# Optimization experiments

Hardware: AMD Instinct MI355X
Metric: run time of the kernel (lower is better)

The kernel has to match this reference:

```python
import jax, jax.numpy as jnp
import numpy as np

N_NODES = 100000
N_EDGES = 1000000
IN_DIM = 64
OUT_DIM = 64
EDGE_DIM = 16
LN_EPS = 1e-5
GINE_EPS = 0.0  # PyG GINEConv default eps


def setup_inputs() -> dict:
    key = jax.random.key(0)
    ks = jax.random.split(key, 10)
    s = lambda d: 1.0 / np.sqrt(d)
    x = jax.random.normal(ks[0], (N_NODES, IN_DIM), dtype=jnp.float32)
    edge_index = jax.random.randint(ks[1], (2, N_EDGES), 0, N_NODES, dtype=jnp.int64)
    edge_attr = jax.random.normal(ks[2], (N_EDGES, EDGE_DIM), dtype=jnp.float32)
    # GINEConv internal edge projection Linear(edge_dim, in_dim)
    We = jax.random.uniform(ks[3], (EDGE_DIM, IN_DIM), jnp.float32, -s(EDGE_DIM), s(EDGE_DIM))
    be = jax.random.uniform(ks[4], (IN_DIM,), jnp.float32, -s(EDGE_DIM), s(EDGE_DIM))
    # MLP: Linear(in_dim, out_dim) -> ReLU -> Linear(out_dim, out_dim)
    W1 = jax.random.uniform(ks[5], (IN_DIM, OUT_DIM), jnp.float32, -s(IN_DIM), s(IN_DIM))
    b1 = jax.random.uniform(ks[6], (OUT_DIM,), jnp.float32, -s(IN_DIM), s(IN_DIM))
    W2 = jax.random.uniform(ks[7], (OUT_DIM, OUT_DIM), jnp.float32, -s(OUT_DIM), s(OUT_DIM))
    b2 = jax.random.uniform(ks[8], (OUT_DIM,), jnp.float32, -s(OUT_DIM), s(OUT_DIM))
    ln_gamma = jnp.ones((OUT_DIM,), jnp.float32)
    ln_beta = jnp.zeros((OUT_DIM,), jnp.float32)
    return {"x": x, "edge_index": edge_index, "edge_attr": edge_attr,
            "We": We, "be": be, "W1": W1, "b1": b1, "W2": W2, "b2": b2,
            "ln_gamma": ln_gamma, "ln_beta": ln_beta}


def reference(x, edge_index, edge_attr, We, be, W1, b1, W2, b2, ln_gamma, ln_beta):
    src, dst = edge_index[0], edge_index[1]
    # message: ReLU(x_j + lin(edge_attr))  [E, IN_DIM]
    msg = jax.nn.relu(x[src] + edge_attr @ We + be)
    # scatter-sum into target nodes  [N, IN_DIM]
    aggr = jax.ops.segment_sum(msg, dst, num_segments=x.shape[0])
    h = (1.0 + GINE_EPS) * x + aggr
    # MLP
    h = jax.nn.relu(h @ W1 + b1) @ W2 + b2
    # LayerNorm over last dim
    mu = jnp.mean(h, axis=-1, keepdims=True)
    var = jnp.var(h, axis=-1, keepdims=True)
    h = (h - mu) * jax.lax.rsqrt(var + LN_EPS) * ln_gamma + ln_beta
    return jax.nn.relu(h)
```

## Files before the change

kernel.cpp:

```cpp
#include <hip/hip_runtime.h>

typedef short short8 __attribute__((ext_vector_type(8)));
typedef float f32x4 __attribute__((ext_vector_type(4)));

__device__ __forceinline__ float bf2f(unsigned short b) {
    union { unsigned u; float f; } c;
    c.u = ((unsigned)b) << 16;
    return c.f;
}

__device__ __forceinline__ unsigned short f2bf(float x) {
    union { float f; unsigned u; } c;
    c.f = x;
    unsigned u = c.u;
    u += 0x7fffu + ((u >> 16) & 1u);
    return (unsigned short)(u >> 16);
}

__device__ __forceinline__ float loadf(const void* p, long long i, unsigned isbf) {
    if (isbf) return bf2f(((const unsigned short*)p)[i]);
    return ((const float*)p)[i];
}

__device__ __forceinline__ f32x4 mfma16(short8 a, short8 b, f32x4 c) {
    return __builtin_amdgcn_mfma_f32_16x16x32_bf16(a, b, c, 0, 0, 0);
}

__global__ void gine_flag_kernel(const unsigned* gm_bits, const unsigned* ei_bits,
                                 unsigned* flags) {
    if (blockIdx.x == 0 && threadIdx.x == 0) {
        flags[0] = (gm_bits[0] == 0x3F803F80u) ? 1u : 0u;
        unsigned o = 0;
        for (int k = 0; k < 8; ++k) o |= ei_bits[2 * k + 1];
        flags[1] = (o == 0u) ? 1u : 0u;
    }
}

__global__ void gine_zero_kernel(float* p, int n) {
    int t = blockIdx.x * blockDim.x + threadIdx.x;
    if (t < n) p[t] = 0.0f;
}

__global__ void gine_prep_kernel(const void* W1, const void* b1,
                                 const void* W2, const void* b2,
                                 const void* gm, const void* bt,
                                 const void* We, const void* be,
                                 const unsigned* flags,
                                 unsigned short* W1B, unsigned short* W2B,
                                 float* vecs) {
    int t = blockIdx.x * blockDim.x + threadIdx.x;
    unsigned isbf = flags[0];
    if (t < 8192) {
        int which = t >> 12;
        int u = t & 4095;
        int j = u & 7, L = (u >> 3) & 63, ktnt = u >> 9;
        int kt = ktnt >> 2, nt = ktnt & 3;
        int k = kt * 32 + (L >> 4) * 8 + j;
        int c = nt * 16 + (L & 15);
        const void* W = which ? W2 : W1;
        unsigned short v = f2bf(loadf(W, k * 64 + c, isbf));
        if (which) W2B[u] = v; else W1B[u] = v;
    } else if (t < 8448) {
        int u = t - 8192;
        const void* s = (u < 64) ? b1 : (u < 128) ? b2 : (u < 192) ? gm : bt;
        vecs[u] = loadf(s, u & 63, isbf);
    } else if (t < 8512) {
        vecs[256 + (t - 8448)] = loadf(be, t - 8448, isbf);
    } else if (t < 9536) {
        int u = t - 8512;
        vecs[320 + u] = loadf(We, u, isbf);
    }
}

__global__ void gine_hist_kernel(const void* edge_index, const unsigned* flags,
                                 int* count, int E, int N) {
    int t = blockIdx.x * blockDim.x + threadIdx.x;
    int stride = gridDim.x * blockDim.x;
    unsigned is64 = flags[1];
    for (int e = t; e < E; e += stride) {
        long long dst = is64 ? ((const long long*)edge_index)[E + e]
                             : (long long)((const int*)edge_index)[E + e];
        if (dst >= 0 && dst < N) atomicAdd(&count[(int)dst], 1);
    }
}

__global__ void gine_scan1_kernel(const int* count, int* row_start, int* bsum,
                                  int N) {
    __shared__ int s[256];
    int t = threadIdx.x;
    int i = blockIdx.x * 256 + t;
    int v = (i < N) ? count[i] : 0;
    s[t] = v;
    __syncthreads();
    for (int off = 1; off < 256; off <<= 1) {
        int u = (t >= off) ? s[t - off] : 0;
        __syncthreads();
        s[t] += u;
        __syncthreads();
    }
    if (i < N) row_start[i] = s[t] - v;
    if (t == 255) bsum[blockIdx.x] = s[255];
}

__global__ void gine_scan2_kernel(int* bsum, int* bscan, int* row_start,
                                  int nb, int N) {
    __shared__ int s[512];
    int t = threadIdx.x;
    int v = (t < nb) ? bsum[t] : 0;
    s[t] = v;
    __syncthreads();
    for (int off = 1; off < 512; off <<= 1) {
        int u = (t >= off) ? s[t - off] : 0;
        __syncthreads();
        s[t] += u;
        __syncthreads();
    }
    if (t < nb) bscan[t] = s[t] - v;
    if (t == nb - 1) row_start[N] = s[t];
}

__global__ void gine_scan3_kernel(int* row_start, int* cursor,
                                  const int* bscan, int N) {
    int i = blockIdx.x * 256 + threadIdx.x;
    if (i < N) {
        int r = row_start[i] + bscan[blockIdx.x];
        row_start[i] = r;
        cursor[i] = r;
    }
}

__global__ void gine_scatter_kernel(const void* edge_index, const unsigned* flags,
                                    int* cursor, unsigned long long* sorted,
                                    int E, int N) {
    int t = blockIdx.x * blockDim.x + threadIdx.x;
    int stride = gridDim.x * blockDim.x;
    unsigned is64 = flags[1];
    for (int e = t; e < E; e += stride) {
        long long src, dst;
        if (is64) {
            src = ((const long long*)edge_index)[e];
            dst = ((const long long*)edge_index)[E + e];
        } else {
            src = ((const int*)edge_index)[e];
            dst = ((const int*)edge_index)[E + e];
        }
        if (dst < 0 || dst >= N) continue;
        if (src < 0) src = 0;
        if (src >= N) src = N - 1;
        int pos = atomicAdd(&cursor[(int)dst], 1);
        sorted[pos] = ((unsigned long long)(unsigned)e << 32) | (unsigned long long)(unsigned)src;
    }
}

__global__ void gine_gather_kernel(const void* x, const void* edge_attr,
                                   const unsigned long long* sorted,
                                   const int* row_start, const float* vecs,
                                   const unsigned* flags, float* h, int N) {
    int w = threadIdx.x >> 6;
    int lane = threadIdx.x & 63;
    int gw = blockIdx.x * 4 + w;
    int nwaves = gridDim.x * 4;
    unsigned isbf = flags[0];

    float Wcol[16];
    for (int k = 0; k < 16; ++k) Wcol[k] = vecs[320 + k * 64 + lane];
    float bev = vecs[256 + lane];

    for (int v = gw; v < N; v += nwaves) {
        float hacc = loadf(x, (long long)v * 64 + lane, isbf);
        int beg = row_start[v];
        int end = row_start[v + 1];
        unsigned long long p = (beg < end) ? sorted[beg] : 0ULL;
        for (int i = beg; i < end; ++i) {
            unsigned long long pn = (i + 1 < end) ? sorted[i + 1] : 0ULL;
            int src = (int)(p & 0xffffffffULL);
            int eid = (int)(p >> 32);

            float xv = loadf(x, (long long)src * 64 + lane, isbf);

            float ea[16];
            if (isbf) {
                const uint4* eap = (const uint4*)((const unsigned short*)edge_attr
                                                  + (size_t)eid * 16);
                uint4 e0 = eap[0];
                uint4 e1 = eap[1];
                unsigned wds[8] = {e0.x, e0.y, e0.z, e0.w, e1.x, e1.y, e1.z, e1.w};
                for (int q = 0; q < 8; ++q) {
                    union { unsigned u; float f; } clo, chi;
                    clo.u = wds[q] << 16;
                    chi.u = wds[q] & 0xffff0000u;
                    ea[2 * q]     = clo.f;
                    ea[2 * q + 1] = chi.f;
                }
            } else {
                const float* eap = (const float*)edge_attr + (size_t)eid * 16;
                for (int q = 0; q < 16; ++q) ea[q] = eap[q];
            }

            float msg = bev;
            for (int k = 0; k < 16; ++k) msg += ea[k] * Wcol[k];
            msg += xv;
            if (msg < 0.f) msg = 0.f;
            hacc += msg;
            p = pn;
        }
        h[(long long)v * 64 + lane] = hacc;
    }
}

__global__ void GINEBlock_49795850830259_kernel(
    const void* x, const void* edge_index, const void* edge_attr,
    const void* We, const void* be, const unsigned* flags,
    float* aggr, int E, int N, int n0, int n1) {
    int wid  = (blockIdx.x * blockDim.x + threadIdx.x) >> 6;
    int lane = threadIdx.x & 63;
    if (wid >= E) return;

    unsigned isbf = flags[0];
    unsigned is64 = flags[1];

    long long src, dst;
    if (is64) {
        src = ((const long long*)edge_index)[wid];
        dst = ((const long long*)edge_index)[E + wid];
    } else {
        src = ((const int*)edge_index)[wid];
        dst = ((const int*)edge_index)[E + wid];
    }
    if (src < 0 || src >= N || dst < n0 || dst >= n1) return;

    float eav = 0.0f;
    if (lane < 16) eav = loadf(edge_attr, (long long)wid * 16 + lane, isbf);

    float acc = loadf(be, lane, isbf);
    for (int k = 0; k < 16; ++k)
        acc += __shfl(eav, k, 64) * loadf(We, k * 64 + lane, isbf);

    acc += loadf(x, src * 64 + lane, isbf);
    if (acc < 0.0f) acc = 0.0f;

    atomicAdd(aggr + (dst - n0) * 64 + lane, acc);
}

__global__ void gine_addx_kernel(const void* x, float* aggr,
                                 const unsigned* flags, int n0, int n1) {
    int t = blockIdx.x * blockDim.x + threadIdx.x;
    int total = (n1 - n0) * 64;
    if (t >= total) return;
    unsigned isbf = flags[0];
    aggr[t] += loadf(x, (long long)n0 * 64 + t, isbf);
}

__global__ __launch_bounds__(256) void gine_node_mfma_kernel(
    const float* h, const unsigned short* W1B, const unsigned short* W2B,
    const float* vecs, const unsigned* flags, void* out, int n0, int n1) {
    __shared__ float Tlds[4][16 * 68];
    int w = threadIdx.x >> 6;
    int L = threadIdx.x & 63;
    int g = L >> 4, m = L & 15;
    int nb = n0 + (blockIdx.x * 4 + w) * 16;
    if (nb >= n1) return;
    unsigned isbf = flags[0];

    const float* b1f = vecs;
    const float* b2f = vecs + 64;
    const float* gmf = vecs + 128;
    const float* btf = vecs + 192;

    int node = nb + m;
    if (node >= n1) node = n1 - 1;
    long long rel = node - n0;

    short8 ahi[2], alo[2];
    for (int kt = 0; kt < 2; ++kt) {
        int fb = kt * 32 + g * 8;
        const float* hp = h + rel * 64 + fb;
        f32x4 a0 = *(const f32x4*)hp;
        f32x4 a1 = *(const f32x4*)(hp + 4);
        for (int j = 0; j < 8; ++j) {
            float hv = (j < 4) ? a0[j] : a1[j - 4];
            unsigned short hb = f2bf(hv);
            float lo = hv - bf2f(hb);
            ahi[kt][j] = (short)hb;
            alo[kt][j] = (short)f2bf(lo);
        }
    }

    float t16[16];
    for (int nt = 0; nt < 4; ++nt) {
        short8 bp0 = *(const short8*)(W1B + ((size_t)(0 * 4 + nt) * 64 + L) * 8);
        short8 bp1 = *(const short8*)(W1B + ((size_t)(1 * 4 + nt) * 64 + L) * 8);
        f32x4 acc = {0.f, 0.f, 0.f, 0.f};
        acc = mfma16(ahi[0], bp0, acc);
        acc = mfma16(ahi[1], bp1, acc);
        acc = mfma16(alo[0], bp0, acc);
        acc = mfma16(alo[1], bp1, acc);
        float bias = b1f[nt * 16 + m];
        for (int r = 0; r < 4; ++r) {
            float v = acc[r] + bias;
            t16[nt * 4 + r] = v > 0.f ? v : 0.f;
        }
    }

    float* tl = Tlds[w];
    for (int nt = 0; nt < 4; ++nt)
        for (int r = 0; r < 4; ++r)
            tl[(g * 4 + r) * 68 + nt * 16 + m] = t16[nt * 4 + r];

    short8 thi[2], tlo[2];
    for (int kt = 0; kt < 2; ++kt) {
        const float* rp = tl + m * 68 + kt * 32 + g * 8;
        f32x4 v0 = *(const f32x4*)rp;
        f32x4 v1 = *(const f32x4*)(rp + 4);
        for (int j = 0; j < 8; ++j) {
            float hv = (j < 4) ? v0[j] : v1[j - 4];
            unsigned short hb = f2bf(hv);
            float lo = hv - bf2f(hb);
            thi[kt][j] = (short)hb;
            tlo[kt][j] = (short)f2bf(lo);
        }
    }

    float o16[16];
    for (int nt = 0; nt < 4; ++nt) {
        short8 bp0 = *(const short8*)(W2B + ((size_t)(0 * 4 + nt) * 64 + L) * 8);
        short8 bp1 = *(const short8*)(W2B + ((size_t)(1 * 4 + nt) * 64 + L) * 8);
        f32x4 acc = {0.f, 0.f, 0.f, 0.f};
        acc = mfma16(thi[0], bp0, acc);
        acc = mfma16(thi[1], bp1, acc);
        acc = mfma16(tlo[0], bp0, acc);
        acc = mfma16(tlo[1], bp1, acc);
        float bias = b2f[nt * 16 + m];
        for (int r = 0; r < 4; ++r) o16[nt * 4 + r] = acc[r] + bias;
    }

    for (int r = 0; r < 4; ++r) {
        float s = o16[r] + o16[4 + r] + o16[8 + r] + o16[12 + r];
        s += __shfl_xor(s, 1, 64);
        s += __shfl_xor(s, 2, 64);
        s += __shfl_xor(s, 4, 64);
        s += __shfl_xor(s, 8, 64);
        float mu = s * (1.0f / 64.0f);
        float v = 0.f;
        for (int nt = 0; nt < 4; ++nt) {
            float d = o16[nt * 4 + r] - mu;
            v += d * d;
        }
        v += __shfl_xor(v, 1, 64);
        v += __shfl_xor(v, 2, 64);
        v += __shfl_xor(v, 4, 64);
        v += __shfl_xor(v, 8, 64);
        float inv = rsqrtf(v * (1.0f / 64.0f) + 1e-5f);
        int nodeR = nb + g * 4 + r;
        if (nodeR < n1) {
            for (int nt = 0; nt < 4; ++nt) {
                int c = nt * 16 + m;
                float rr = (o16[nt * 4 + r] - mu) * inv * gmf[c] + btf[c];
                if (rr < 0.f) rr = 0.f;
                long long oidx = (long long)nodeR * 64 + c;
                if (isbf) ((unsigned short*)out)[oidx] = f2bf(rr);
                else      ((float*)out)[oidx] = rr;
            }
        }
    }
}

static inline size_t align256(size_t a) { return (a + 255) & ~(size_t)255; }

extern "C" void kernel_launch(void* const* d_in, const int* in_sizes, int n_in,
                              void* d_out, int out_size, void* d_ws, size_t ws_size,
                              hipStream_t stream) {
    const void* x          = d_in[0];
    const void* edge_index = d_in[1];
    const void* edge_attr  = d_in[2];
    const void* We         = d_in[3];
    const void* be         = d_in[4];
    const void* W1         = d_in[5];
    const void* b1         = d_in[6];
    const void* W2         = d_in[7];
    const void* b2         = d_in[8];
    const void* gm         = d_in[9];
    const void* bt         = d_in[10];

    const int N = in_sizes[0] / 64;
    const int E = in_sizes[1] / 2;

    unsigned* flags     = (unsigned*)d_ws;
    unsigned short* W1B = (unsigned short*)((char*)d_ws + 256);
    unsigned short* W2B = W1B + 4096;
    float* vecs         = (float*)(W2B + 4096);
    int* bsum           = (int*)((char*)d_ws + 24576);
    int* bscan          = bsum + 1024;

    gine_flag_kernel<<<1, 64, 0, stream>>>((const unsigned*)gm,
                                           (const unsigned*)edge_index, flags);
    gine_prep_kernel<<<38, 256, 0, stream>>>(W1, b1, W2, b2, gm, bt, We, be,
                                             flags, W1B, W2B, vecs);

    size_t o_count  = 32768;
    size_t o_row    = o_count + align256((size_t)N * 4);
    size_t o_cursor = o_row + align256((size_t)(N + 1) * 4);
    size_t o_sorted = o_cursor + align256((size_t)N * 4);
    size_t o_h      = o_sorted + align256((size_t)E * 8);
    size_t need     = o_h + (size_t)N * 256;

    int nb = (N + 255) / 256;

    if (ws_size >= need && nb <= 512) {
        int* count    = (int*)((char*)d_ws + o_count);
        int* row_start= (int*)((char*)d_ws + o_row);
        int* cursor   = (int*)((char*)d_ws + o_cursor);
        unsigned long long* sorted = (unsigned long long*)((char*)d_ws + o_sorted);
        float* h      = (float*)((char*)d_ws + o_h);

        gine_zero_kernel<<<(N + 255) / 256, 256, 0, stream>>>((float*)count, N);
        gine_hist_kernel<<<1024, 256, 0, stream>>>(edge_index, flags, count, E, N);
        gine_scan1_kernel<<<nb, 256, 0, stream>>>(count, row_start, bsum, N);
        gine_scan2_kernel<<<1, 512, 0, stream>>>(bsum, bscan, row_start, nb, N);
        gine_scan3_kernel<<<nb, 256, 0, stream>>>(row_start, cursor, bscan, N);
        gine_scatter_kernel<<<1024, 256, 0, stream>>>(edge_index, flags, cursor,
                                                      sorted, E, N);
        int gblocks = (N + 15) / 16;
        if (gblocks > 6250) gblocks = 6250;
        gine_gather_kernel<<<gblocks, 256, 0, stream>>>(x, edge_attr, sorted,
                                                        row_start, vecs, flags, h, N);
        int node_blocks = (N + 63) / 64;
        gine_node_mfma_kernel<<<node_blocks, 256, 0, stream>>>(
            h, W1B, W2B, vecs, flags, d_out, 0, N);
        return;
    }

    float* aggr = (float*)((char*)d_ws + 32768);
    long long usable = (ws_size > 32768) ? (long long)(ws_size - 32768) : 0;
    long long ncll = (usable / 256) & ~63LL;
    int NC = (ncll > N) ? N : (int)ncll;
    if (NC < 64) return;

    long long edge_threads = (long long)E * 64;
    int edge_blocks = (int)((edge_threads + 255) / 256);

    for (int n0 = 0; n0 < N; n0 += NC) {
        int n1 = n0 + NC; if (n1 > N) n1 = N;
        int chunk = n1 - n0;
        int n_aggr = chunk * 64;

        gine_zero_kernel<<<(n_aggr + 255) / 256, 256, 0, stream>>>(aggr, n_aggr);
        GINEBlock_49795850830259_kernel<<<edge_blocks, 256, 0, stream>>>(
            x, edge_index, edge_attr, We, be, flags, aggr, E, N, n0, n1);
        gine_addx_kernel<<<(n_aggr + 255) / 256, 256, 0, stream>>>(
            x, aggr, flags, n0, n1);
        int node_blocks = (chunk + 63) / 64;
        gine_node_mfma_kernel<<<node_blocks, 256, 0, stream>>>(
            aggr, W1B, W2B, vecs, flags, d_out, n0, n1);
    }
}
```

Measured before the change: 474.7 us.

## Compute edge messages in edge order into CSR slots, then segment-sum per node

Adds a new primary path that computes each edge message in edge order (coalesced reads of edge_attr and edge_index) and writes the full 64-float message into a dst-sorted slot obtained via atomic cursor. A second kernel then sums contiguous messages per node with x added. This replaces the scatter-of-indices plus gather path that read edge_attr randomly. In exchange it writes and rereads a 256 MB message buffer, and the new path only runs if the workspace is large enough.

```diff
diff --git a/kernel.cpp b/kernel.cpp
--- a/kernel.cpp
+++ b/kernel.cpp
@@ -129,6 +129,99 @@
     }
 }
 
+__global__ void gine_edgemsg_kernel(const void* x, const void* edge_index,
+                                    const void* edge_attr, const float* vecs,
+                                    const unsigned* flags, int* cursor,
+                                    float* msg, int E, int N) {
+    int w = threadIdx.x >> 6;
+    int lane = threadIdx.x & 63;
+    int gw = blockIdx.x * (blockDim.x >> 6) + w;
+    int nw = gridDim.x * (blockDim.x >> 6);
+    unsigned isbf = flags[0];
+    unsigned is64 = flags[1];
+
+    float Wcol[16];
+    #pragma unroll
+    for (int k = 0; k < 16; ++k) Wcol[k] = vecs[320 + k * 64 + lane];
+    float bev = vecs[256 + lane];
+
+    for (int e = gw; e < E; e += nw) {
+        long long src, dst;
+        if (is64) {
+            src = ((const long long*)edge_index)[e];
+            dst = ((const long long*)edge_index)[E + e];
+        } else {
+            src = ((const int*)edge_index)[e];
+            dst = ((const int*)edge_index)[E + e];
+        }
+        if (dst < 0 || dst >= N) continue;
+        if (src < 0) src = 0;
+        if (src >= N) src = N - 1;
+
+        int pos = 0;
+        if (lane == 0) pos = atomicAdd(&cursor[(int)dst], 1);
+        pos = __shfl(pos, 0, 64);
+
+        float xv = loadf(x, src * 64 + lane, isbf);
+
+        float acc = bev;
+        if (isbf) {
+            const uint4* eap = (const uint4*)((const unsigned short*)edge_attr
+                                              + (size_t)e * 16);
+            uint4 e0 = eap[0];
+            uint4 e1 = eap[1];
+            unsigned wds[8] = {e0.x, e0.y, e0.z, e0.w, e1.x, e1.y, e1.z, e1.w};
+            #pragma unroll
+            for (int q = 0; q < 8; ++q) {
+                union { unsigned u; float f; } clo, chi;
+                clo.u = wds[q] << 16;
+                chi.u = wds[q] & 0xffff0000u;
+                acc += clo.f * Wcol[2 * q] + chi.f * Wcol[2 * q + 1];
+            }
+        } else {
+            const f32x4* eap = (const f32x4*)((const float*)edge_attr
+                                              + (size_t)e * 16);
+            f32x4 e0 = eap[0], e1 = eap[1], e2 = eap[2], e3 = eap[3];
+            float ea[16] = {e0[0], e0[1], e0[2], e0[3],
+                            e1[0], e1[1], e1[2], e1[3],
+                            e2[0], e2[1], e2[2], e2[3],
+                            e3[0], e3[1], e3[2], e3[3]};
+            #pragma unroll
+            for (int k = 0; k < 16; ++k) acc += ea[k] * Wcol[k];
+        }
+        acc += xv;
+        if (acc < 0.f) acc = 0.f;
+        msg[(size_t)pos * 64 + lane] = acc;
+    }
+}
+
+__global__ void gine_sum_kernel(const void* x, const float* msg,
+                                const int* row_start, const unsigned* flags,
+                                float* h, int N) {
+    int w = threadIdx.x >> 6;
+    int lane = threadIdx.x & 63;
+    int gw = blockIdx.x * 4 + w;
+    int nwaves = gridDim.x * 4;
+    unsigned isbf = flags[0];
+    for (int v = gw; v < N; v += nwaves) {
+        int beg = row_start[v];
+        int end = row_start[v + 1];
+        float a0 = loadf(x, (long long)v * 64 + lane, isbf);
+        float a1 = 0.f, a2 = 0.f, a3 = 0.f;
+        int p = beg;
+        for (; p + 4 <= end; p += 4) {
+            const float* mp = msg + (size_t)p * 64 + lane;
+            float m0 = mp[0];
+            float m1 = mp[64];
+            float m2 = mp[128];
+            float m3 = mp[192];
+            a0 += m0; a1 += m1; a2 += m2; a3 += m3;
+        }
+        for (; p < end; ++p) a0 += msg[(size_t)p * 64 + lane];
+        h[(long long)v * 64 + lane] = (a0 + a1) + (a2 + a3);
+    }
+}
+
 __global__ void gine_scatter_kernel(const void* edge_index, const unsigned* flags,
                                     int* cursor, unsigned long long* sorted,
                                     int E, int N) {
@@ -397,14 +490,48 @@
     gine_prep_kernel<<<38, 256, 0, stream>>>(W1, b1, W2, b2, gm, bt, We, be,
                                              flags, W1B, W2B, vecs);
 
+    int nb = (N + 255) / 256;
+    int node_blocks = (N + 63) / 64;
+    int gblocks = (N + 15) / 16;
+    if (gblocks > 6250) gblocks = 6250;
+
+    {
+        size_t a_count  = 32768;
+        size_t a_row    = a_count + align256((size_t)N * 4);
+        size_t a_cursor = a_row + align256((size_t)(N + 1) * 4);
+        size_t a_msg    = a_cursor + align256((size_t)N * 4);
+        size_t a_h      = a_msg + align256((size_t)E * 256);
+        size_t needA    = a_h + (size_t)N * 256;
+
+        if (ws_size >= needA && nb <= 512) {
+            int* count     = (int*)((char*)d_ws + a_count);
+            int* row_start = (int*)((char*)d_ws + a_row);
+            int* cursor    = (int*)((char*)d_ws + a_cursor);
+            float* msg     = (float*)((char*)d_ws + a_msg);
+            float* h       = (float*)((char*)d_ws + a_h);
+
+            gine_zero_kernel<<<(N + 255) / 256, 256, 0, stream>>>((float*)count, N);
+            gine_hist_kernel<<<1024, 256, 0, stream>>>(edge_index, flags, count, E, N);
+            gine_scan1_kernel<<<nb, 256, 0, stream>>>(count, row_start, bsum, N);
+            gine_scan2_kernel<<<1, 512, 0, stream>>>(bsum, bscan, row_start, nb, N);
+            gine_scan3_kernel<<<nb, 256, 0, stream>>>(row_start, cursor, bscan, N);
+            gine_edgemsg_kernel<<<4096, 256, 0, stream>>>(x, edge_index, edge_attr,
+                                                          vecs, flags, cursor,
+                                                          msg, E, N);
+            gine_sum_kernel<<<gblocks, 256, 0, stream>>>(x, msg, row_start,
+                                                         flags, h, N);
+            gine_node_mfma_kernel<<<node_blocks, 256, 0, stream>>>(
+                h, W1B, W2B, vecs, flags, d_out, 0, N);
+            return;
+        }
+    }
+
     size_t o_count  = 32768;
     size_t o_row    = o_count + align256((size_t)N * 4);
     size_t o_cursor = o_row + align256((size_t)(N + 1) * 4);
     size_t o_sorted = o_cursor + align256((size_t)N * 4);
     size_t o_h      = o_sorted + align256((size_t)E * 8);
     size_t need     = o_h + (size_t)N * 256;
-
-    int nb = (N + 255) / 256;
 
     if (ws_size >= need && nb <= 512) {
         int* count    = (int*)((char*)d_ws + o_count);
@@ -420,11 +547,8 @@
         gine_scan3_kernel<<<nb, 256, 0, stream>>>(row_start, cursor, bscan, N);
         gine_scatter_kernel<<<1024, 256, 0, stream>>>(edge_index, flags, cursor,
                                                       sorted, E, N);
-        int gblocks = (N + 15) / 16;
-        if (gblocks > 6250) gblocks = 6250;
         gine_gather_kernel<<<gblocks, 256, 0, stream>>>(x, edge_attr, sorted,
                                                         row_start, vecs, flags, h, N);
-        int node_blocks = (N + 63) / 64;
         gine_node_mfma_kernel<<<node_blocks, 256, 0, stream>>>(
             h, W1B, W2B, vecs, flags, d_out, 0, N);
         return;
@@ -449,8 +573,8 @@
             x, edge_index, edge_attr, We, be, flags, aggr, E, N, n0, n1);
         gine_addx_kernel<<<(n_aggr + 255) / 256, 256, 0, stream>>>(
             x, aggr, flags, n0, n1);
-        int node_blocks = (chunk + 63) / 64;
-        gine_node_mfma_kernel<<<node_blocks, 256, 0, stream>>>(
+        int chunk_blocks = (chunk + 63) / 64;
+        gine_node_mfma_kernel<<<chunk_blocks, 256, 0, stream>>>(
             aggr, W1B, W2B, vecs, flags, d_out, n0, n1);
     }
 }
```

New measurement: 466.7 us. Within noise of the previous version (-1.7%).
